# Kernel tuning notes

Measured on AMD Instinct MI355X. Metric: run time of the kernel, lower is better.

## Reference

```python
import jax, jax.numpy as jnp
import numpy as np
from jax import lax

COM, INP, HID, OUT = 128, 512, 2048, 512
T = 16384
SCALE = 35.0  # softmax temperature from the original code


def setup_inputs() -> dict:
    key = jax.random.key(0)
    ks = jax.random.split(key, 10)
    d_in = INP + COM          # 640
    d_out = OUT + COM         # 640
    s1 = 1.0 / np.sqrt(d_in)
    s2 = 1.0 / np.sqrt(HID)
    return {
        "I1": jax.random.normal(ks[0], (T, INP), dtype=jnp.float32),
        "I2": jax.random.normal(ks[1], (T, INP), dtype=jnp.float32),
        "A1W1_w": jax.random.uniform(ks[2], (HID, d_in), jnp.float32, -s1, s1),
        "A1W1_b": jax.random.uniform(ks[3], (HID,), jnp.float32, -s1, s1),
        "A1W2_w": jax.random.uniform(ks[4], (d_out, HID), jnp.float32, -s2, s2),
        "A1W2_b": jax.random.uniform(ks[5], (d_out,), jnp.float32, -s2, s2),
        "A2W1_w": jax.random.uniform(ks[6], (HID, d_in), jnp.float32, -s1, s1),
        "A2W1_b": jax.random.uniform(ks[7], (HID,), jnp.float32, -s1, s1),
        "A2W2_w": jax.random.uniform(ks[8], (d_out, HID), jnp.float32, -s2, s2),
        "A2W2_b": jax.random.uniform(ks[9], (d_out,), jnp.float32, -s2, s2),
    }


def reference(I1, I2, A1W1_w, A1W1_b, A1W2_w, A1W2_b, A2W1_w, A2W1_b, A2W2_w, A2W2_b):
    lrelu = jax.nn.leaky_relu  # negative_slope=0.01, matches torch default
    i1 = I1[0]  # only row 0 is ever used, as in the original forward
    i2 = I2[0]

    def agent1(m2):
        x = jnp.concatenate([i1, m2])
        return lrelu(lrelu(x @ A1W1_w.T + A1W1_b) @ A1W2_w.T + A1W2_b)

    def agent2(m1):
        x = jnp.concatenate([i2, m1])
        return lrelu(lrelu(x @ A2W1_w.T + A2W1_b) @ A2W2_w.T + A2W2_b)

    def step(carry, t):
        sum_c1, sum_c2 = carry  # running sums of com1/com2 rows
        denom = (t + 1).astype(jnp.float32)
        # mean of com2[:t+1]; row t is still zero here (matches torch in-place semantics)
        m2a = sum_c2 / denom
        com1 = jax.nn.softmax(SCALE * agent1(m2a)[OUT:])
        sum_c1 = sum_c1 + com1
        m1 = sum_c1 / denom  # com1[t] now included
        full2 = agent2(m1)
        out2 = full2[:OUT]
        com2 = jax.nn.softmax(SCALE * full2[OUT:])
        sum_c2 = sum_c2 + com2
        m2b = sum_c2 / denom  # com2[t] now included
        out1 = agent1(m2b)[:OUT]
        return (sum_c1, sum_c2), (out1, out2)

    init = (jnp.zeros(COM, jnp.float32), jnp.zeros(COM, jnp.float32))
    _, (out1, out2) = lax.scan(step, init, jnp.arange(I1.shape[0]))
    return out1, out2  # each [T, OUT]
```

## Files before the change

kernel.cpp:

```cpp
#include <hip/hip_runtime.h>
#include <hip/hip_bf16.h>

#define T_STEPS 16384
#define COMD 128
#define INPD 512
#define HIDD 2048
#define OUTD 512
#define DIN 640
#define SCALE_F 35.0f
#define NTEAM 32
#define HS 64

using u16 = unsigned short;
using u32 = unsigned int;

__device__ __forceinline__ float lrelu(float x){ return x >= 0.f ? x : 0.01f*x; }
__device__ __forceinline__ float bf2f(u16 u){ return __uint_as_float(((u32)u)<<16); }
__device__ __forceinline__ u16 f2bf(float f){ u32 x = __float_as_uint(f); return (u16)((x + 0x7fffu + ((x>>16)&1u)) >> 16); }

__global__ void __launch_bounds__(256) prep_base_kernel(
    const float* __restrict__ I1, const float* __restrict__ I2,
    const float* __restrict__ W11, const float* __restrict__ b11,
    const float* __restrict__ W21, const float* __restrict__ b21,
    float* __restrict__ base)
{
  int row = blockIdx.x*4 + (threadIdx.x>>6);
  int lane = threadIdx.x & 63;
  int agent = row >> 11;
  int h = row & 2047;
  const float* W  = agent ? W21 : W11;
  const float* in = agent ? I2  : I1;
  const float* bv = agent ? b21 : b11;
  float acc = 0.f;
  #pragma unroll
  for (int k = 0; k < 8; ++k)
    acc += W[(size_t)h*DIN + k*64 + lane] * in[k*64 + lane];
  #pragma unroll
  for (int off = 32; off; off >>= 1) acc += __shfl_xor(acc, off);
  if (lane == 0) base[agent*HIDD + h] = acc + bv[h];
}

__global__ void __launch_bounds__(256) cvt_kernel(
    const float* __restrict__ W12, const float* __restrict__ W22,
    u16* __restrict__ o1, u16* __restrict__ o2)
{
  size_t i = ((size_t)blockIdx.x*256 + threadIdx.x)*4;
  float4 a = *reinterpret_cast<const float4*>(W12 + i);
  float4 b = *reinterpret_cast<const float4*>(W22 + i);
  ushort4 ua = { f2bf(a.x), f2bf(a.y), f2bf(a.z), f2bf(a.w) };
  ushort4 ub = { f2bf(b.x), f2bf(b.y), f2bf(b.z), f2bf(b.w) };
  *reinterpret_cast<ushort4*>(o1 + i) = ua;
  *reinterpret_cast<ushort4*>(o2 + i) = ub;
}

__device__ __forceinline__ void softmax128(const int tid, float* s_z, float* s_red, float* s_com)
{
  if (tid < COMD) {
    float m = s_z[tid];
    #pragma unroll
    for (int off = 32; off; off >>= 1) m = fmaxf(m, __shfl_xor(m, off));
    if ((tid & 63) == 0) s_red[tid>>6] = m;
  }
  __syncthreads();
  float M = fmaxf(s_red[0], s_red[1]);
  float e = 0.f;
  if (tid < COMD) e = __expf(s_z[tid] - M);
  float ssum = e;
  #pragma unroll
  for (int off = 32; off; off >>= 1) ssum += __shfl_xor(ssum, off);
  if (tid < COMD && (tid & 63) == 0) s_red[4 + (tid>>6)] = ssum;
  __syncthreads();
  if (tid < COMD) s_com[tid] = e / (s_red[4] + s_red[5]);
  __syncthreads();
}

__global__ void __launch_bounds__(512, 1) team_kernel(
    const float* __restrict__ W11, const float* __restrict__ W21,
    const float* __restrict__ W12, const float* __restrict__ W22,
    const float* __restrict__ b12, const float* __restrict__ b22,
    const float* __restrict__ base,
    float* __restrict__ P1, float* __restrict__ P2, u32* __restrict__ cnts,
    void* __restrict__ hist1, void* __restrict__ hist2, int hf32)
{
  __shared__ float sWa1[HS*129];
  __shared__ float sWa2[HS*129];
  __shared__ float sU1[COMD*65];
  __shared__ float sU2[COMD*65];
  __shared__ float s_b1[HS], s_b2[HS], s_w[HS], s_v[HS], s_h1a[HS], s_h2[HS];
  __shared__ float s_bc1[COMD], s_bc2[COMD], s_com[COMD], s_z[COMD];
  __shared__ float s_lp[512];
  __shared__ float s_red[8];

  const int g = blockIdx.x;
  const int tid = threadIdx.x;
  const int h0 = g*HS;

  for (int idx = tid; idx < HS*COMD; idx += 512) {
    int h = idx >> 7, c = idx & 127;
    sWa1[h*129+c] = W11[(size_t)(h0+h)*DIN + INPD + c];
    sWa2[h*129+c] = W21[(size_t)(h0+h)*DIN + INPD + c];
  }
  for (int idx = tid; idx < COMD*HS; idx += 512) {
    int o = idx >> 6, h = idx & 63;
    sU1[o*65+h] = W12[(size_t)(OUTD+o)*HIDD + h0 + h];
    sU2[o*65+h] = W22[(size_t)(OUTD+o)*HIDD + h0 + h];
  }
  if (tid < COMD) { s_bc1[tid] = b12[OUTD+tid]; s_bc2[tid] = b22[OUTD+tid]; }
  if (tid < HS)   { s_b1[tid] = base[h0+tid]; s_b2[tid] = base[HIDD+h0+tid]; s_w[tid]=0.f; s_v[tid]=0.f; }
  __syncthreads();

  float* h1f = (float*)hist1; u16* h1u = (u16*)hist1;
  float* h2f = (float*)hist2; u16* h2u = (u16*)hist2;

  for (int t = 0; t < T_STEPS; ++t) {
    const float invd = 1.f/(float)(t+1);

    if (tid < HS) s_h1a[tid] = lrelu(s_b1[tid] + s_w[tid]*invd);
    __syncthreads();

    {
      int r = tid >> 7, o = tid & 127;
      const float* Up = &sU1[o*65 + r*16];
      const float* hp = &s_h1a[r*16];
      float acc = 0.f;
      #pragma unroll
      for (int j = 0; j < 16; ++j) acc += Up[j]*hp[j];
      s_lp[tid] = acc;
    }
    __syncthreads();
    if (tid < COMD) {
      float pl = s_lp[tid] + s_lp[COMD+tid] + s_lp[2*COMD+tid] + s_lp[3*COMD+tid];
      __hip_atomic_store(&P1[g*COMD + tid], pl, __ATOMIC_RELAXED, __HIP_MEMORY_SCOPE_AGENT);
    }
    __syncthreads();
    if (tid == 0) {
      __hip_atomic_fetch_add(&cnts[0], 1u, __ATOMIC_RELEASE, __HIP_MEMORY_SCOPE_AGENT);
      while (__hip_atomic_load(&cnts[0], __ATOMIC_ACQUIRE, __HIP_MEMORY_SCOPE_AGENT) < (u32)(NTEAM*(t+1))) {}
    }
    __syncthreads();
    {
      int o = tid & 127, grp = tid >> 7;
      float s = 0.f;
      #pragma unroll
      for (int j = 0; j < 8; ++j)
        s += __hip_atomic_load(&P1[(grp*8+j)*COMD + o], __ATOMIC_RELAXED, __HIP_MEMORY_SCOPE_AGENT);
      s_lp[tid] = s;
    }
    __syncthreads();
    if (tid < COMD) {
      float d = s_lp[tid]+s_lp[COMD+tid]+s_lp[2*COMD+tid]+s_lp[3*COMD+tid] + s_bc1[tid];
      s_z[tid] = SCALE_F * lrelu(d);
    }
    __syncthreads();
    softmax128(tid, s_z, s_red, s_com);

    {
      int w = tid >> 6, lane = tid & 63;
      const float* Wp = &sWa2[lane*129 + w*16];
      const float* cp = &s_com[w*16];
      float acc = 0.f;
      #pragma unroll
      for (int j = 0; j < 16; ++j) acc += Wp[j]*cp[j];
      s_lp[tid] = acc;
    }
    __syncthreads();
    if (tid < HS) {
      float s = s_v[tid];
      #pragma unroll
      for (int w = 0; w < 8; ++w) s += s_lp[w*64 + tid];
      s_v[tid] = s;
      float x = lrelu(s_b2[tid] + s*invd);
      s_h2[tid] = x;
      if (hf32) h2f[(size_t)t*HIDD + h0 + tid] = x; else h2u[(size_t)t*HIDD + h0 + tid] = f2bf(x);
    }
    __syncthreads();

    {
      int r = tid >> 7, o = tid & 127;
      const float* Up = &sU2[o*65 + r*16];
      const float* hp = &s_h2[r*16];
      float acc = 0.f;
      #pragma unroll
      for (int j = 0; j < 16; ++j) acc += Up[j]*hp[j];
      s_lp[tid] = acc;
    }
    __syncthreads();
    if (tid < COMD) {
      float pl = s_lp[tid] + s_lp[COMD+tid] + s_lp[2*COMD+tid] + s_lp[3*COMD+tid];
      __hip_atomic_store(&P2[g*COMD + tid], pl, __ATOMIC_RELAXED, __HIP_MEMORY_SCOPE_AGENT);
    }
    __syncthreads();
    if (tid == 0) {
      __hip_atomic_fetch_add(&cnts[1], 1u, __ATOMIC_RELEASE, __HIP_MEMORY_SCOPE_AGENT);
      while (__hip_atomic_load(&cnts[1], __ATOMIC_ACQUIRE, __HIP_MEMORY_SCOPE_AGENT) < (u32)(NTEAM*(t+1))) {}
    }
    __syncthreads();
    {
      int o = tid & 127, grp = tid >> 7;
      float s = 0.f;
      #pragma unroll
      for (int j = 0; j < 8; ++j)
        s += __hip_atomic_load(&P2[(grp*8+j)*COMD + o], __ATOMIC_RELAXED, __HIP_MEMORY_SCOPE_AGENT);
      s_lp[tid] = s;
    }
    __syncthreads();
    if (tid < COMD) {
      float d = s_lp[tid]+s_lp[COMD+tid]+s_lp[2*COMD+tid]+s_lp[3*COMD+tid] + s_bc2[tid];
      s_z[tid] = SCALE_F * lrelu(d);
    }
    __syncthreads();
    softmax128(tid, s_z, s_red, s_com);

    {
      int w = tid >> 6, lane = tid & 63;
      const float* Wp = &sWa1[lane*129 + w*16];
      const float* cp = &s_com[w*16];
      float acc = 0.f;
      #pragma unroll
      for (int j = 0; j < 16; ++j) acc += Wp[j]*cp[j];
      s_lp[tid] = acc;
    }
    __syncthreads();
    if (tid < HS) {
      float s = s_w[tid];
      #pragma unroll
      for (int w = 0; w < 8; ++w) s += s_lp[w*64 + tid];
      s_w[tid] = s;
      float x = lrelu(s_b1[tid] + s*invd);
      if (hf32) h1f[(size_t)t*HIDD + h0 + tid] = x; else h1u[(size_t)t*HIDD + h0 + tid] = f2bf(x);
    }
    __syncthreads();
  }
}

__global__ void __launch_bounds__(256) out_kernel(
    const void* __restrict__ hist1, const void* __restrict__ hist2,
    const u16* __restrict__ Wb1, const u16* __restrict__ Wb2,
    const float* __restrict__ b12, const float* __restrict__ b22,
    float* __restrict__ out, int hf32)
{
  __shared__ float hl[8][2048];
  const int head = blockIdx.x & 1;
  const int t0 = (blockIdx.x >> 1) * 8;
  const int tid = threadIdx.x;
  const void* hist = head ? hist2 : hist1;
  const u16* W = head ? Wb2 : Wb1;
  const float* bias = head ? b22 : b12;
  float* op = out + (size_t)head * T_STEPS * OUTD;

  if (hf32) {
    const float* hf = (const float*)hist;
    for (int idx = tid; idx < 8*2048; idx += 256)
      hl[idx>>11][idx&2047] = hf[(size_t)t0*HIDD + idx];
  } else {
    const u16* hu = (const u16*)hist;
    for (int idx = tid; idx < 8*2048; idx += 256)
      hl[idx>>11][idx&2047] = bf2f(hu[(size_t)t0*HIDD + idx]);
  }
  __syncthreads();

  const int wave = tid >> 6, lane = tid & 63;
  for (int row = wave; row < OUTD; row += 4) {
    const u16* wr = W + (size_t)row*HIDD;
    float acc[8] = {0,0,0,0,0,0,0,0};
    #pragma unroll
    for (int k = 0; k < 8; ++k) {
      const int e = k*256 + lane*4;
      uint2 pw = *reinterpret_cast<const uint2*>(wr + e);
      float w0 = bf2f((u16)(pw.x & 0xffffu));
      float w1 = bf2f((u16)(pw.x >> 16));
      float w2 = bf2f((u16)(pw.y & 0xffffu));
      float w3 = bf2f((u16)(pw.y >> 16));
      #pragma unroll
      for (int tt = 0; tt < 8; ++tt) {
        const float4 hv = *reinterpret_cast<const float4*>(&hl[tt][e]);
        acc[tt] += w0*hv.x + w1*hv.y + w2*hv.z + w3*hv.w;
      }
    }
    #pragma unroll
    for (int tt = 0; tt < 8; ++tt) {
      float a = acc[tt];
      #pragma unroll
      for (int off = 32; off; off >>= 1) a += __shfl_xor(a, off);
      acc[tt] = a;
    }
    if (lane == 0) {
      const float b = bias[row];
      #pragma unroll
      for (int tt = 0; tt < 8; ++tt)
        op[(size_t)(t0+tt)*OUTD + row] = lrelu(acc[tt] + b);
    }
  }
}

extern "C" void kernel_launch(void* const* d_in, const int* in_sizes, int n_in,
                              void* d_out, int out_size, void* d_ws, size_t ws_size,
                              hipStream_t stream)
{
  const float* I1  = (const float*)d_in[0];
  const float* I2  = (const float*)d_in[1];
  const float* W11 = (const float*)d_in[2];
  const float* b11 = (const float*)d_in[3];
  const float* W12 = (const float*)d_in[4];
  const float* b12 = (const float*)d_in[5];
  const float* W21 = (const float*)d_in[6];
  const float* b21 = (const float*)d_in[7];
  const float* W22 = (const float*)d_in[8];
  const float* b22 = (const float*)d_in[9];

  char* ws = (char*)d_ws;
  float* base = (float*)ws;
  float* P1 = (float*)(ws + 16384);
  float* P2 = (float*)(ws + 32768);
  u32* cnts = (u32*)(ws + 49152);
  char* hist1 = ws + 65536;
  const size_t histF = (size_t)T_STEPS*HIDD*4;
  const size_t histU = (size_t)T_STEPS*HIDD*2;
  const size_t wbB   = (size_t)OUTD*HIDD*2;
  const size_t needF = 65536 + 2*histF + 2*wbB;
  int hf32 = (ws_size >= needF) ? 1 : 0;
  const size_t hb = hf32 ? histF : histU;
  char* hist2 = hist1 + hb;
  u16* Wb1 = (u16*)(hist2 + hb);
  u16* Wb2 = Wb1 + (size_t)OUTD*HIDD;

  hipMemsetAsync(cnts, 0, 256, stream);
  prep_base_kernel<<<1024, 256, 0, stream>>>(I1, I2, W11, b11, W21, b21, base);
  cvt_kernel<<<1024, 256, 0, stream>>>(W12, W22, Wb1, Wb2);

  void* h1v = (void*)hist1; void* h2v = (void*)hist2;
  void* kargs[] = { (void*)&W11, (void*)&W21, (void*)&W12, (void*)&W22,
                    (void*)&b12, (void*)&b22, (void*)&base,
                    (void*)&P1, (void*)&P2, (void*)&cnts,
                    (void*)&h1v, (void*)&h2v, (void*)&hf32 };
  hipLaunchCooperativeKernel((const void*)team_kernel, dim3(NTEAM), dim3(512),
                             kargs, 0, stream);

  out_kernel<<<(T_STEPS/8)*2, 256, 0, stream>>>(h1v, h2v, Wb1, Wb2, b12, b22,
                                                (float*)d_out, hf32);
}
```

Baseline: 127.3 ms.

## Split team into per-agent workgroup groups with flag-based producer/consumer sync

Instead of every one of 32 workgroups handling a 64-wide hidden slice of both agents, 16 workgroups now own 128 hidden units of agent1 and 16 own agent2. Each group publishes partial logits plus a per-workgroup step flag, and the other group polls only those flags. This replaces the two global atomic-counter barriers per step with point-to-point release/acquire flags and fuses the softmax into a single wave. The aim is to cut barrier latency and the number of __syncthreads on the serial critical path. In exchange each workgroup does twice the per-step dot-product work, and the two groups now alternate between working and waiting.

After: 121.7 ms. -4.4%, faster.

```diff
diff --git a/kernel.cpp b/kernel.cpp
--- a/kernel.cpp
+++ b/kernel.cpp
@@ -8,8 +8,8 @@
 #define OUTD 512
 #define DIN 640
 #define SCALE_F 35.0f
-#define NTEAM 32
-#define HS 64
+#define NA 16
+#define HSA 128
 
 using u16 = unsigned short;
 using u32 = unsigned int;
@@ -53,183 +53,131 @@
   *reinterpret_cast<ushort4*>(o2 + i) = ub;
 }
 
-__device__ __forceinline__ void softmax128(const int tid, float* s_z, float* s_red, float* s_com)
-{
-  if (tid < COMD) {
-    float m = s_z[tid];
-    #pragma unroll
-    for (int off = 32; off; off >>= 1) m = fmaxf(m, __shfl_xor(m, off));
-    if ((tid & 63) == 0) s_red[tid>>6] = m;
-  }
-  __syncthreads();
-  float M = fmaxf(s_red[0], s_red[1]);
-  float e = 0.f;
-  if (tid < COMD) e = __expf(s_z[tid] - M);
-  float ssum = e;
-  #pragma unroll
-  for (int off = 32; off; off >>= 1) ssum += __shfl_xor(ssum, off);
-  if (tid < COMD && (tid & 63) == 0) s_red[4 + (tid>>6)] = ssum;
-  __syncthreads();
-  if (tid < COMD) s_com[tid] = e / (s_red[4] + s_red[5]);
-  __syncthreads();
-}
-
 __global__ void __launch_bounds__(512, 1) team_kernel(
     const float* __restrict__ W11, const float* __restrict__ W21,
     const float* __restrict__ W12, const float* __restrict__ W22,
     const float* __restrict__ b12, const float* __restrict__ b22,
     const float* __restrict__ base,
-    float* __restrict__ P1, float* __restrict__ P2, u32* __restrict__ cnts,
+    float* __restrict__ P1, float* __restrict__ P2,
+    u32* __restrict__ F1, u32* __restrict__ F2,
     void* __restrict__ hist1, void* __restrict__ hist2, int hf32)
 {
-  __shared__ float sWa1[HS*129];
-  __shared__ float sWa2[HS*129];
-  __shared__ float sU1[COMD*65];
-  __shared__ float sU2[COMD*65];
-  __shared__ float s_b1[HS], s_b2[HS], s_w[HS], s_v[HS], s_h1a[HS], s_h2[HS];
-  __shared__ float s_bc1[COMD], s_bc2[COMD], s_com[COMD], s_z[COMD];
+  __shared__ float sWa[HSA][129];
+  __shared__ float sU[COMD][129];
+  __shared__ float s_b[HSA], s_st[HSA], s_h[HSA];
+  __shared__ float s_bc[COMD], s_com[COMD];
   __shared__ float s_lp[512];
-  __shared__ float s_red[8];
-
-  const int g = blockIdx.x;
+
+  const int wg = blockIdx.x;
+  const bool isA1 = (wg < NA);
+  const int g = isA1 ? wg : wg - NA;
+  const int h0 = g * HSA;
   const int tid = threadIdx.x;
-  const int h0 = g*HS;
-
-  for (int idx = tid; idx < HS*COMD; idx += 512) {
+
+  const float* W1  = isA1 ? W11 : W21;
+  const float* W2  = isA1 ? W12 : W22;
+  const float* bL2 = isA1 ? b12 : b22;
+  const float* bs  = base + (isA1 ? 0 : HIDD);
+  float* Pout = isA1 ? P1 : P2;
+  float* Pin  = isA1 ? P2 : P1;
+  u32*   Fout = isA1 ? F1 : F2;
+  u32*   Fin  = isA1 ? F2 : F1;
+  void*  hist = isA1 ? hist1 : hist2;
+  float* histf = (float*)hist; u16* histu = (u16*)hist;
+
+  for (int idx = tid; idx < HSA*COMD; idx += 512) {
     int h = idx >> 7, c = idx & 127;
-    sWa1[h*129+c] = W11[(size_t)(h0+h)*DIN + INPD + c];
-    sWa2[h*129+c] = W21[(size_t)(h0+h)*DIN + INPD + c];
-  }
-  for (int idx = tid; idx < COMD*HS; idx += 512) {
-    int o = idx >> 6, h = idx & 63;
-    sU1[o*65+h] = W12[(size_t)(OUTD+o)*HIDD + h0 + h];
-    sU2[o*65+h] = W22[(size_t)(OUTD+o)*HIDD + h0 + h];
-  }
-  if (tid < COMD) { s_bc1[tid] = b12[OUTD+tid]; s_bc2[tid] = b22[OUTD+tid]; }
-  if (tid < HS)   { s_b1[tid] = base[h0+tid]; s_b2[tid] = base[HIDD+h0+tid]; s_w[tid]=0.f; s_v[tid]=0.f; }
+    sWa[h][c] = W1[(size_t)(h0+h)*DIN + INPD + c];
+  }
+  for (int idx = tid; idx < COMD*HSA; idx += 512) {
+    int o = idx >> 7, h = idx & 127;
+    sU[o][h] = W2[(size_t)(OUTD+o)*HIDD + h0 + h];
+  }
+  if (tid < COMD) s_bc[tid] = bL2[OUTD + tid];
+  if (tid < HSA) { s_b[tid] = bs[h0 + tid]; s_st[tid] = 0.f; }
   __syncthreads();
 
-  float* h1f = (float*)hist1; u16* h1u = (u16*)hist1;
-  float* h2f = (float*)hist2; u16* h2u = (u16*)hist2;
-
   for (int t = 0; t < T_STEPS; ++t) {
-    const float invd = 1.f/(float)(t+1);
-
-    if (tid < HS) s_h1a[tid] = lrelu(s_b1[tid] + s_w[tid]*invd);
-    __syncthreads();
-
-    {
-      int r = tid >> 7, o = tid & 127;
-      const float* Up = &sU1[o*65 + r*16];
-      const float* hp = &s_h1a[r*16];
+    const float invd = 1.f / (float)(t+1);
+
+    if (isA1) {
+      if (tid < HSA) s_h[tid] = lrelu(s_b[tid] + s_st[tid]*invd);
+      __syncthreads();
+      { int o = tid & 127, r = tid >> 7;
+        const float* hp = &s_h[r*32];
+        float acc = 0.f;
+        #pragma unroll
+        for (int j = 0; j < 32; ++j) acc += sU[o][r*32+j] * hp[j];
+        s_lp[tid] = acc; }
+      __syncthreads();
+      if (tid < COMD) {
+        float p = s_lp[tid]+s_lp[128+tid]+s_lp[256+tid]+s_lp[384+tid];
+        __hip_atomic_store(&Pout[g*COMD+tid], p, __ATOMIC_RELAXED, __HIP_MEMORY_SCOPE_AGENT);
+      }
+      __syncthreads();
+      if (tid == 0)
+        __hip_atomic_store(&Fout[g*16], (u32)(t+1), __ATOMIC_RELEASE, __HIP_MEMORY_SCOPE_AGENT);
+    }
+
+    if (tid < NA) {
+      while (__hip_atomic_load(&Fin[tid*16], __ATOMIC_ACQUIRE, __HIP_MEMORY_SCOPE_AGENT) < (u32)(t+1)) {}
+    }
+    __syncthreads();
+    { int o = tid & 127, p4 = tid >> 7;
+      float s = 0.f;
+      #pragma unroll
+      for (int j = 0; j < 4; ++j)
+        s += __hip_atomic_load(&Pin[(p4*4+j)*COMD + o], __ATOMIC_RELAXED, __HIP_MEMORY_SCOPE_AGENT);
+      s_lp[tid] = s; }
+    __syncthreads();
+    if (tid < 64) {
+      int o0 = tid, o1 = tid + 64;
+      float z0 = SCALE_F * lrelu(s_lp[o0]+s_lp[128+o0]+s_lp[256+o0]+s_lp[384+o0] + s_bc[o0]);
+      float z1 = SCALE_F * lrelu(s_lp[o1]+s_lp[128+o1]+s_lp[256+o1]+s_lp[384+o1] + s_bc[o1]);
+      float m = fmaxf(z0, z1);
+      #pragma unroll
+      for (int off = 32; off; off >>= 1) m = fmaxf(m, __shfl_xor(m, off));
+      float e0 = __expf(z0 - m), e1 = __expf(z1 - m);
+      float s = e0 + e1;
+      #pragma unroll
+      for (int off = 32; off; off >>= 1) s += __shfl_xor(s, off);
+      float r = 1.f / s;
+      s_com[o0] = e0 * r; s_com[o1] = e1 * r;
+    }
+    __syncthreads();
+    { int h = tid & 127, q = tid >> 7;
+      const float* cp = &s_com[q*32];
       float acc = 0.f;
       #pragma unroll
-      for (int j = 0; j < 16; ++j) acc += Up[j]*hp[j];
-      s_lp[tid] = acc;
-    }
-    __syncthreads();
-    if (tid < COMD) {
-      float pl = s_lp[tid] + s_lp[COMD+tid] + s_lp[2*COMD+tid] + s_lp[3*COMD+tid];
-      __hip_atomic_store(&P1[g*COMD + tid], pl, __ATOMIC_RELAXED, __HIP_MEMORY_SCOPE_AGENT);
-    }
-    __syncthreads();
-    if (tid == 0) {
-      __hip_atomic_fetch_add(&cnts[0], 1u, __ATOMIC_RELEASE, __HIP_MEMORY_SCOPE_AGENT);
-      while (__hip_atomic_load(&cnts[0], __ATOMIC_ACQUIRE, __HIP_MEMORY_SCOPE_AGENT) < (u32)(NTEAM*(t+1))) {}
-    }
-    __syncthreads();
-    {
-      int o = tid & 127, grp = tid >> 7;
-      float s = 0.f;
-      #pragma unroll
-      for (int j = 0; j < 8; ++j)
-        s += __hip_atomic_load(&P1[(grp*8+j)*COMD + o], __ATOMIC_RELAXED, __HIP_MEMORY_SCOPE_AGENT);
-      s_lp[tid] = s;
-    }
-    __syncthreads();
-    if (tid < COMD) {
-      float d = s_lp[tid]+s_lp[COMD+tid]+s_lp[2*COMD+tid]+s_lp[3*COMD+tid] + s_bc1[tid];
-      s_z[tid] = SCALE_F * lrelu(d);
-    }
-    __syncthreads();
-    softmax128(tid, s_z, s_red, s_com);
-
-    {
-      int w = tid >> 6, lane = tid & 63;
-      const float* Wp = &sWa2[lane*129 + w*16];
-      const float* cp = &s_com[w*16];
-      float acc = 0.f;
-      #pragma unroll
-      for (int j = 0; j < 16; ++j) acc += Wp[j]*cp[j];
-      s_lp[tid] = acc;
-    }
-    __syncthreads();
-    if (tid < HS) {
-      float s = s_v[tid];
-      #pragma unroll
-      for (int w = 0; w < 8; ++w) s += s_lp[w*64 + tid];
-      s_v[tid] = s;
-      float x = lrelu(s_b2[tid] + s*invd);
-      s_h2[tid] = x;
-      if (hf32) h2f[(size_t)t*HIDD + h0 + tid] = x; else h2u[(size_t)t*HIDD + h0 + tid] = f2bf(x);
-    }
-    __syncthreads();
-
-    {
-      int r = tid >> 7, o = tid & 127;
-      const float* Up = &sU2[o*65 + r*16];
-      const float* hp = &s_h2[r*16];
-      float acc = 0.f;
-      #pragma unroll
-      for (int j = 0; j < 16; ++j) acc += Up[j]*hp[j];
-      s_lp[tid] = acc;
-    }
-    __syncthreads();
-    if (tid < COMD) {
-      float pl = s_lp[tid] + s_lp[COMD+tid] + s_lp[2*COMD+tid] + s_lp[3*COMD+tid];
-      __hip_atomic_store(&P2[g*COMD + tid], pl, __ATOMIC_RELAXED, __HIP_MEMORY_SCOPE_AGENT);
-    }
-    __syncthreads();
-    if (tid == 0) {
-      __hip_atomic_fetch_add(&cnts[1], 1u, __ATOMIC_RELEASE, __HIP_MEMORY_SCOPE_AGENT);
-      while (__hip_atomic_load(&cnts[1], __ATOMIC_ACQUIRE, __HIP_MEMORY_SCOPE_AGENT) < (u32)(NTEAM*(t+1))) {}
-    }
-    __syncthreads();
-    {
-      int o = tid & 127, grp = tid >> 7;
-      float s = 0.f;
-      #pragma unroll
-      for (int j = 0; j < 8; ++j)
-        s += __hip_atomic_load(&P2[(grp*8+j)*COMD + o], __ATOMIC_RELAXED, __HIP_MEMORY_SCOPE_AGENT);
-      s_lp[tid] = s;
-    }
-    __syncthreads();
-    if (tid < COMD) {
-      float d = s_lp[tid]+s_lp[COMD+tid]+s_lp[2*COMD+tid]+s_lp[3*COMD+tid] + s_bc2[tid];
-      s_z[tid] = SCALE_F * lrelu(d);
-    }
-    __syncthreads();
-    softmax128(tid, s_z, s_red, s_com);
-
-    {
-      int w = tid >> 6, lane = tid & 63;
-      const float* Wp = &sWa1[lane*129 + w*16];
-      const float* cp = &s_com[w*16];
-      float acc = 0.f;
-      #pragma unroll
-      for (int j = 0; j < 16; ++j) acc += Wp[j]*cp[j];
-      s_lp[tid] = acc;
-    }
-    __syncthreads();
-    if (tid < HS) {
-      float s = s_w[tid];
-      #pragma unroll
-      for (int w = 0; w < 8; ++w) s += s_lp[w*64 + tid];
-      s_w[tid] = s;
-      float x = lrelu(s_b1[tid] + s*invd);
-      if (hf32) h1f[(size_t)t*HIDD + h0 + tid] = x; else h1u[(size_t)t*HIDD + h0 + tid] = f2bf(x);
-    }
-    __syncthreads();
+      for (int j = 0; j < 32; ++j) acc += sWa[h][q*32+j] * cp[j];
+      s_lp[tid] = acc; }
+    __syncthreads();
+    if (tid < HSA) {
+      float st = s_st[tid] + s_lp[tid]+s_lp[128+tid]+s_lp[256+tid]+s_lp[384+tid];
+      s_st[tid] = st;
+      float x = lrelu(s_b[tid] + st*invd);
+      s_h[tid] = x;
+      if (hf32) histf[(size_t)t*HIDD + h0 + tid] = x;
+      else      histu[(size_t)t*HIDD + h0 + tid] = f2bf(x);
+    }
+
+    if (!isA1) {
+      __syncthreads();
+      { int o = tid & 127, r = tid >> 7;
+        const float* hp = &s_h[r*32];
+        float acc = 0.f;
+        #pragma unroll
+        for (int j = 0; j < 32; ++j) acc += sU[o][r*32+j] * hp[j];
+        s_lp[tid] = acc; }
+      __syncthreads();
+      if (tid < COMD) {
+        float p = s_lp[tid]+s_lp[128+tid]+s_lp[256+tid]+s_lp[384+tid];
+        __hip_atomic_store(&Pout[g*COMD+tid], p, __ATOMIC_RELAXED, __HIP_MEMORY_SCOPE_AGENT);
+      }
+      __syncthreads();
+      if (tid == 0)
+        __hip_atomic_store(&Fout[g*16], (u32)(t+1), __ATOMIC_RELEASE, __HIP_MEMORY_SCOPE_AGENT);
+    }
   }
 }
 
@@ -312,7 +260,8 @@
   float* base = (float*)ws;
   float* P1 = (float*)(ws + 16384);
   float* P2 = (float*)(ws + 32768);
-  u32* cnts = (u32*)(ws + 49152);
+  u32* F1 = (u32*)(ws + 49152);
+  u32* F2 = (u32*)(ws + 53248);
   char* hist1 = ws + 65536;
   const size_t histF = (size_t)T_STEPS*HIDD*4;
   const size_t histU = (size_t)T_STEPS*HIDD*2;
@@ -324,16 +273,16 @@
   u16* Wb1 = (u16*)(hist2 + hb);
   u16* Wb2 = Wb1 + (size_t)OUTD*HIDD;
 
-  hipMemsetAsync(cnts, 0, 256, stream);
+  hipMemsetAsync(ws + 49152, 0, 8192, stream);
   prep_base_kernel<<<1024, 256, 0, stream>>>(I1, I2, W11, b11, W21, b21, base);
   cvt_kernel<<<1024, 256, 0, stream>>>(W12, W22, Wb1, Wb2);
 
   void* h1v = (void*)hist1; void* h2v = (void*)hist2;
   void* kargs[] = { (void*)&W11, (void*)&W21, (void*)&W12, (void*)&W22,
                     (void*)&b12, (void*)&b22, (void*)&base,
-                    (void*)&P1, (void*)&P2, (void*)&cnts,
+                    (void*)&P1, (void*)&P2, (void*)&F1, (void*)&F2,
                     (void*)&h1v, (void*)&h2v, (void*)&hf32 };
-  hipLaunchCooperativeKernel((const void*)team_kernel, dim3(NTEAM), dim3(512),
+  hipLaunchCooperativeKernel((const void*)team_kernel, dim3(2*NA), dim3(512),
                              kargs, 0, stream);
 
   out_kernel<<<(T_STEPS/8)*2, 256, 0, stream>>>(h1v, h2v, Wb1, Wb2, b12, b22,
```
